# Performance work log

Measured on AMD Instinct MI355X. Metric: run time of the kernel, lower is better.

The kernel has to match this reference:

```python
import jax, jax.numpy as jnp
import numpy as np

N, E, H, ED = 20000, 640000, 128, 16


def _lin_init(k, fan_in, fan_out):
    kw, kb = jax.random.split(k)
    lim = 1.0 / np.sqrt(fan_in)
    W = jax.random.uniform(kw, (fan_in, fan_out), jnp.float32, -lim, lim)
    b = jax.random.uniform(kb, (fan_out,), jnp.float32, -lim, lim)
    return W, b


def setup_inputs() -> dict:
    key = jax.random.key(0)
    ks = jax.random.split(key, 12)
    h = jax.random.normal(ks[0], (N, H), jnp.float32)
    x = jax.random.normal(ks[1], (N, 3), jnp.float32)
    edge_index = jax.random.randint(ks[2], (2, E), 0, N, jnp.int32)
    edge_attr = jax.random.normal(ks[3], (E, ED), jnp.float32)
    fixed_mask = jax.random.randint(ks[4], (N,), 0, 2, jnp.int32).astype(bool)
    We1, be1 = _lin_init(ks[5], 2 * H + 1 + ED, H)
    We2, be2 = _lin_init(ks[6], H, H)
    Wx1, bx1 = _lin_init(ks[7], H, H)
    Wx2, bx2 = _lin_init(ks[8], H, 1)
    Wh1, bh1 = _lin_init(ks[9], 2 * H, H)
    Wh2, bh2 = _lin_init(ks[10], H, H)
    return {"h": h, "x": x, "edge_index": edge_index, "edge_attr": edge_attr,
            "fixed_mask": fixed_mask,
            "We1": We1, "be1": be1, "We2": We2, "be2": be2,
            "Wx1": Wx1, "bx1": bx1, "Wx2": Wx2, "bx2": bx2,
            "Wh1": Wh1, "bh1": bh1, "Wh2": Wh2, "bh2": bh2}


def reference(h, x, edge_index, edge_attr, fixed_mask,
              We1, be1, We2, be2, Wx1, bx1, Wx2, bx2, Wh1, bh1, Wh2, bh2):
    src, dst = edge_index[0], edge_index[1]
    n = h.shape[0]
    diff = x[src] - x[dst]                               # [E,3]
    dist_sq_norm = jnp.sum(diff * diff, -1, keepdims=True) / 100.0
    e_in = jnp.concatenate([h[src], h[dst], dist_sq_norm, edge_attr], -1)
    m_ij = jax.nn.silu(jax.nn.silu(e_in @ We1 + be1) @ We2 + be2)  # [E,H]
    coord_w = jnp.tanh(jax.nn.silu(m_ij @ Wx1 + bx1) @ Wx2 + bx2)  # [E,1]
    coord_agg = jax.ops.segment_sum(diff * coord_w, dst, num_segments=n)
    coord_agg = coord_agg * (~fixed_mask).astype(h.dtype)[:, None]
    msg_agg = jax.ops.segment_sum(m_ij, dst, num_segments=n)       # [N,H]
    h_new = h + jax.nn.silu(jnp.concatenate([h, msg_agg], -1) @ Wh1 + bh1) @ Wh2 + bh2
    x_new = x + coord_agg
    return h_new, x_new
```

## Files before the change

kernel.cpp:

```cpp
#include <hip/hip_runtime.h>
#include <hip/hip_bf16.h>
#include <math.h>

#define NN   20000
#define NE   640000
#define HD   128
#define EDIM 16
#define KIN  273
#define P2   136

#define S_PWT   4096
#define S_PWE1M 32768
#define S_PW4   16384
#define S_PWH1  32768
#define S_PWH2  16384

typedef __bf16 bf16x8 __attribute__((ext_vector_type(8)));
typedef float  f32x4  __attribute__((ext_vector_type(4)));

__device__ __forceinline__ float silu_f(float v) {
    const float e = __expf(-v);
    return v * __builtin_amdgcn_rcpf(1.0f + e);
}
__device__ __forceinline__ float tanh_f(float s) {
    const float e = __expf(2.0f * s);
    return 1.0f - 2.0f * __builtin_amdgcn_rcpf(e + 1.0f);
}
__device__ __forceinline__ unsigned short f2bf(float f) {
    __bf16 b = (__bf16)f;
    return __builtin_bit_cast(unsigned short, b);
}
__device__ __forceinline__ float bf2f(unsigned short u) {
    __bf16 b = __builtin_bit_cast(__bf16, u);
    return (float)b;
}
__device__ __forceinline__ unsigned pack2bf(float a, float b) {
    return (unsigned)f2bf(a) | ((unsigned)f2bf(b) << 16);
}

__device__ __forceinline__ void pack_id(const float* __restrict__ W, int Kreal,
                                        unsigned short* __restrict__ P, int idx) {
    const int f = idx >> 9, r = idx & 511;
    const int lane = r >> 3, j = r & 7;
    const int kb = f >> 3, nb = f & 7;
    const int k = kb * 32 + (lane >> 4) * 8 + j;
    const int n = nb * 16 + (lane & 15);
    P[idx] = f2bf((k < Kreal) ? W[(size_t)k * HD + n] : 0.0f);
}
__device__ __forceinline__ void pack_il(const float* __restrict__ W, int Kreal,
                                        unsigned short* __restrict__ P, int idx) {
    const int f = idx >> 9, r = idx & 511;
    const int lane = r >> 3, j = r & 7;
    const int kb = f >> 3, nb = f & 7;
    const int k = kb * 32 + (lane >> 4) * 8 + j;
    const int n = (nb >> 1) * 32 + 2 * (lane & 15) + (nb & 1);
    P[idx] = f2bf((k < Kreal) ? W[(size_t)k * HD + n] : 0.0f);
}

#define ZDW (NN*(HD+3))

__global__ void egnn_prep_kernel(
    const float* __restrict__ h, const int* __restrict__ ei,
    const float* __restrict__ We1, const float* __restrict__ We2,
    const float* __restrict__ Wx1, const float* __restrict__ Wh1,
    const float* __restrict__ Wh2,
    int* __restrict__ zbase,
    unsigned short* __restrict__ hb,
    unsigned short* __restrict__ PWt,  unsigned short* __restrict__ PWe1m,
    unsigned short* __restrict__ PWe2, unsigned short* __restrict__ PWx1,
    unsigned short* __restrict__ PWh1, unsigned short* __restrict__ PWh2,
    int* __restrict__ cnt)
{
    const size_t NH4 = (size_t)NN * HD / 4;
    const size_t Z1 = ZDW, C1 = Z1 + NH4;
    const size_t T1 = C1 + S_PWT, T2 = T1 + S_PWE1M, T3 = T2 + S_PW4;
    const size_t T4 = T3 + S_PW4, T5 = T4 + S_PWH1, T6 = T5 + S_PWH2;
    const size_t TOT = T6 + NE;
    const size_t stride = (size_t)gridDim.x * blockDim.x;
    for (size_t i = (size_t)blockIdx.x * blockDim.x + threadIdx.x; i < TOT; i += stride) {
        if (i < Z1) { zbase[i] = 0; continue; }
        if (i < C1) {
            const size_t r = i - Z1;
            const float4 v = ((const float4*)h)[r];
            unsigned* dst = (unsigned*)&hb[r * 4];
            dst[0] = pack2bf(v.x, v.y);
            dst[1] = pack2bf(v.z, v.w);
            continue;
        }
        if (i < T1) {
            const int idx = (int)(i - C1);
            const int r = idx & 511, nb = idx >> 9;
            const int lane = r >> 3, j = r & 7;
            const int k = 256 + (lane >> 4) * 8 + j;
            const int n = (nb >> 1) * 32 + 2 * (lane & 15) + (nb & 1);
            PWt[idx] = f2bf((k < KIN) ? We1[(size_t)k * HD + n] : 0.0f);
            continue;
        }
        if (i < T2) { pack_il(We1, 256, PWe1m, (int)(i - T1)); continue; }
        if (i < T3) { pack_il(We2, HD, PWe2, (int)(i - T2)); continue; }
        if (i < T4) { pack_il(Wx1, HD, PWx1, (int)(i - T3)); continue; }
        if (i < T5) { pack_id(Wh1, 2 * HD, PWh1, (int)(i - T4)); continue; }
        if (i < T6) { pack_id(Wh2, HD, PWh2, (int)(i - T5)); continue; }
        atomicAdd(&cnt[ei[NE + (i - T6)]], 1);
    }
}

__global__ __launch_bounds__(256, 4) void egnn_pre_kernel(
    const unsigned short* __restrict__ hb,
    const unsigned short* __restrict__ PWe1m, const float* __restrict__ be1,
    const int* __restrict__ cnt, int* __restrict__ cursor,
    unsigned short* __restrict__ preS, unsigned short* __restrict__ preD)
{
    const int t = threadIdx.x;
    if (blockIdx.x == 313) {
        __shared__ int ls[256];
        const int base = t * 79;
        int c[79];
        int s = 0;
        for (int i = 0; i < 79; ++i) {
            const int idx = base + i;
            c[i] = (idx < NN) ? cnt[idx] : 0;
            s += c[i];
        }
        ls[t] = s;
        __syncthreads();
        int v = s;
        for (int off = 1; off < 256; off <<= 1) {
            const int u = (t >= off) ? ls[t - off] : 0;
            __syncthreads();
            v += u;
            ls[t] = v;
            __syncthreads();
        }
        int run = v - s;
        for (int i = 0; i < 79; ++i) {
            const int idx = base + i;
            if (idx < NN) { cursor[idx] = run; run += c[i]; }
        }
        return;
    }
    const int n0 = blockIdx.x * 64;
    const int lane = t & 63, w = t >> 6;
    const int quad = lane >> 4, l16 = lane & 15;
    int arow[4];
    #pragma unroll
    for (int mb = 0; mb < 4; ++mb) arow[mb] = min(n0 + mb * 16 + l16, NN - 1);

    f32x4 accS[4][2], accD[4][2];
    #pragma unroll
    for (int mb = 0; mb < 4; ++mb)
        #pragma unroll
        for (int nt = 0; nt < 2; ++nt) {
            accS[mb][nt] = (f32x4){0.f,0.f,0.f,0.f};
            accD[mb][nt] = (f32x4){0.f,0.f,0.f,0.f};
        }
    #pragma unroll
    for (int kb = 0; kb < 4; ++kb) {
        bf16x8 a[4], bS[2], bD[2];
        #pragma unroll
        for (int mb = 0; mb < 4; ++mb)
            a[mb] = *(const bf16x8*)&hb[(size_t)arow[mb] * HD + kb * 32 + quad * 8];
        #pragma unroll
        for (int nt = 0; nt < 2; ++nt) {
            bS[nt] = *(const bf16x8*)&PWe1m[((kb * 8 + w * 2 + nt) * 64 + lane) * 8];
            bD[nt] = *(const bf16x8*)&PWe1m[(((4 + kb) * 8 + w * 2 + nt) * 64 + lane) * 8];
        }
        #pragma unroll
        for (int mb = 0; mb < 4; ++mb)
            #pragma unroll
            for (int nt = 0; nt < 2; ++nt) {
                accS[mb][nt] = __builtin_amdgcn_mfma_f32_16x16x32_bf16(
                    a[mb], bS[nt], accS[mb][nt], 0, 0, 0);
                accD[mb][nt] = __builtin_amdgcn_mfma_f32_16x16x32_bf16(
                    a[mb], bD[nt], accD[mb][nt], 0, 0, 0);
            }
    }
    const int cb = w * 32 + 2 * l16;
    const float2 b1 = *(const float2*)&be1[cb];
    #pragma unroll
    for (int mb = 0; mb < 4; ++mb)
        #pragma unroll
        for (int r = 0; r < 4; ++r) {
            const int n = n0 + mb * 16 + quad * 4 + r;
            if (n < NN) {
                *(unsigned*)&preS[(size_t)n * HD + cb] =
                    pack2bf(accS[mb][0][r], accS[mb][1][r]);
                *(unsigned*)&preD[(size_t)n * HD + cb] =
                    pack2bf(accD[mb][0][r] + b1.x, accD[mb][1][r] + b1.y);
            }
        }
}

__global__ void egnn_perm_kernel(const int* __restrict__ ei,
                                 int* __restrict__ cursor, int* __restrict__ perm) {
    const int e = blockIdx.x * 256 + threadIdx.x;
    const int pos = atomicAdd(&cursor[ei[NE + e]], 1);
    perm[pos] = e;
}

__global__ __launch_bounds__(256, 4) void egnn_edge_kernel(
    const unsigned short* __restrict__ preS, const unsigned short* __restrict__ preD,
    const float* __restrict__ x,
    const int* __restrict__ ei, const float* __restrict__ eattr,
    const int* __restrict__ perm,
    const unsigned short* __restrict__ PWt,
    const unsigned short* __restrict__ PWe2, const float* __restrict__ be2,
    const unsigned short* __restrict__ PWx1, const float* __restrict__ bx1,
    const float* __restrict__ Wx2, const float* __restrict__ bx2,
    float* __restrict__ msg_agg, float* __restrict__ coord_agg)
{
    __shared__ __align__(16) unsigned short tail[64 * 32];
    __shared__ __align__(16) unsigned short sT[64 * P2];
    __shared__ __align__(16) unsigned short sM[64 * P2];
    __shared__ int   sE[64], sSrc[64], sDst[64];
    __shared__ float sDiff[64][3];
    __shared__ float sW[64];

    const int t  = threadIdx.x;
    const int e0 = blockIdx.x * 64;

    if (t < 64) {
        const int e = perm[e0 + t];
        sE[t] = e;
        const int s = ei[e];
        const int d = ei[NE + e];
        sSrc[t] = s; sDst[t] = d;
        const float dx = x[s*3+0] - x[d*3+0];
        const float dy = x[s*3+1] - x[d*3+1];
        const float dz = x[s*3+2] - x[d*3+2];
        sDiff[t][0] = dx; sDiff[t][1] = dy; sDiff[t][2] = dz;
        tail[t * 32 + 0] = f2bf((dx*dx + dy*dy + dz*dz) * 0.01f);
    }
    __syncthreads();

    const int lane = t & 63;
    const int w    = t >> 6;
    const int quad = lane >> 4;
    const int l16  = lane & 15;
    const int cb   = w * 32 + 2 * l16;

    f32x4 preC[4][2];
    #pragma unroll
    for (int mb = 0; mb < 4; ++mb)
        #pragma unroll
        for (int r = 0; r < 4; ++r) {
            const int row = mb * 16 + quad * 4 + r;
            const unsigned us = *(const unsigned*)&preS[(size_t)sSrc[row] * HD + cb];
            const unsigned ud = *(const unsigned*)&preD[(size_t)sDst[row] * HD + cb];
            preC[mb][0][r] = bf2f((unsigned short)(us & 0xffff)) +
                             bf2f((unsigned short)(ud & 0xffff));
            preC[mb][1][r] = bf2f((unsigned short)(us >> 16)) +
                             bf2f((unsigned short)(ud >> 16));
        }

    {
        const int eL = t >> 2, q = t & 3;
        const int eG = sE[eL];
        #pragma unroll
        for (int jj = 0; jj < 8; ++jj) {
            const int col = q * 8 + jj;
            if (col == 0) continue;
            float v = 0.0f;
            if (col <= EDIM) v = eattr[(size_t)eG * EDIM + (col - 1)];
            tail[eL * 32 + col] = f2bf(v);
        }
    }
    __syncthreads();

    f32x4 acc1[4][2];
    {
        bf16x8 a[4], b[2];
        #pragma unroll
        for (int mb = 0; mb < 4; ++mb)
            a[mb] = *(const bf16x8*)&tail[(mb * 16 + l16) * 32 + quad * 8];
        #pragma unroll
        for (int nt = 0; nt < 2; ++nt)
            b[nt] = *(const bf16x8*)&PWt[((w * 2 + nt) * 64 + lane) * 8];
        #pragma unroll
        for (int mb = 0; mb < 4; ++mb)
            #pragma unroll
            for (int nt = 0; nt < 2; ++nt)
                acc1[mb][nt] = __builtin_amdgcn_mfma_f32_16x16x32_bf16(
                    a[mb], b[nt], preC[mb][nt], 0, 0, 0);
    }
    #pragma unroll
    for (int mb = 0; mb < 4; ++mb)
        #pragma unroll
        for (int r = 0; r < 4; ++r) {
            const int row = mb * 16 + quad * 4 + r;
            *(unsigned*)&sT[row * P2 + cb] =
                pack2bf(silu_f(acc1[mb][0][r]), silu_f(acc1[mb][1][r]));
        }
    __syncthreads();

    f32x4 acc2[4][2];
    #pragma unroll
    for (int mb = 0; mb < 4; ++mb)
        #pragma unroll
        for (int nt = 0; nt < 2; ++nt) acc2[mb][nt] = (f32x4){0.f,0.f,0.f,0.f};
    #pragma unroll
    for (int kb = 0; kb < 4; ++kb) {
        bf16x8 a[4], b[2];
        #pragma unroll
        for (int mb = 0; mb < 4; ++mb)
            a[mb] = *(const bf16x8*)&sT[(mb * 16 + l16) * P2 + kb * 32 + quad * 8];
        #pragma unroll
        for (int nt = 0; nt < 2; ++nt)
            b[nt] = *(const bf16x8*)&PWe2[((kb * 8 + w * 2 + nt) * 64 + lane) * 8];
        #pragma unroll
        for (int mb = 0; mb < 4; ++mb)
            #pragma unroll
            for (int nt = 0; nt < 2; ++nt)
                acc2[mb][nt] = __builtin_amdgcn_mfma_f32_16x16x32_bf16(
                    a[mb], b[nt], acc2[mb][nt], 0, 0, 0);
    }
    {
        const float2 b2 = *(const float2*)&be2[cb];
        #pragma unroll
        for (int mb = 0; mb < 4; ++mb)
            #pragma unroll
            for (int r = 0; r < 4; ++r) {
                const int row = mb * 16 + quad * 4 + r;
                *(unsigned*)&sM[row * P2 + cb] =
                    pack2bf(silu_f(acc2[mb][0][r] + b2.x),
                            silu_f(acc2[mb][1][r] + b2.y));
            }
    }
    __syncthreads();

    {
        const int cp = t & 63;
        const int r0 = (t >> 6) * 16;
        float a0 = 0.0f, a1 = 0.0f;
        #pragma unroll 4
        for (int r = 0; r < 16; ++r) {
            const int row = r0 + r;
            const int d   = sDst[row];
            const unsigned u = *(const unsigned*)&sM[row * P2 + 2 * cp];
            a0 += bf2f((unsigned short)(u & 0xffff));
            a1 += bf2f((unsigned short)(u >> 16));
            const bool flush = (r == 15) || (sDst[row + 1] != d);
            if (flush) {
                atomicAdd(&msg_agg[(size_t)d * HD + 2 * cp], a0);
                atomicAdd(&msg_agg[(size_t)d * HD + 2 * cp + 1], a1);
                a0 = 0.0f; a1 = 0.0f;
            }
        }
    }

    f32x4 acc3[4][2];
    #pragma unroll
    for (int mb = 0; mb < 4; ++mb)
        #pragma unroll
        for (int nt = 0; nt < 2; ++nt) acc3[mb][nt] = (f32x4){0.f,0.f,0.f,0.f};
    #pragma unroll
    for (int kb = 0; kb < 4; ++kb) {
        bf16x8 a[4], b[2];
        #pragma unroll
        for (int mb = 0; mb < 4; ++mb)
            a[mb] = *(const bf16x8*)&sM[(mb * 16 + l16) * P2 + kb * 32 + quad * 8];
        #pragma unroll
        for (int nt = 0; nt < 2; ++nt)
            b[nt] = *(const bf16x8*)&PWx1[((kb * 8 + w * 2 + nt) * 64 + lane) * 8];
        #pragma unroll
        for (int mb = 0; mb < 4; ++mb)
            #pragma unroll
            for (int nt = 0; nt < 2; ++nt)
                acc3[mb][nt] = __builtin_amdgcn_mfma_f32_16x16x32_bf16(
                    a[mb], b[nt], acc3[mb][nt], 0, 0, 0);
    }
    {
        const float2 bx = *(const float2*)&bx1[cb];
        const float2 w2 = *(const float2*)&Wx2[cb];
        float p[4][4];
        #pragma unroll
        for (int mb = 0; mb < 4; ++mb)
            #pragma unroll
            for (int r = 0; r < 4; ++r)
                p[mb][r] = silu_f(acc3[mb][0][r] + bx.x) * w2.x +
                           silu_f(acc3[mb][1][r] + bx.y) * w2.y;
        #pragma unroll
        for (int off = 8; off >= 1; off >>= 1)
            #pragma unroll
            for (int mb = 0; mb < 4; ++mb)
                #pragma unroll
                for (int r = 0; r < 4; ++r)
                    p[mb][r] += __shfl_xor(p[mb][r], off, 64);
        if (l16 == 0) {
            float* red = reinterpret_cast<float*>(sT);
            #pragma unroll
            for (int mb = 0; mb < 4; ++mb)
                #pragma unroll
                for (int r = 0; r < 4; ++r)
                    red[w * 64 + mb * 16 + quad * 4 + r] = p[mb][r];
        }
    }
    __syncthreads();
    if (t < 64) {
        const float* red = reinterpret_cast<const float*>(sT);
        sW[t] = tanh_f(red[t] + red[64 + t] + red[128 + t] + red[192 + t] + bx2[0]);
    }
    __syncthreads();

    if (w < 3) {
        const int dstv = sDst[lane];
        float v = sDiff[lane][w] * sW[lane];
        #pragma unroll
        for (int off = 1; off <= 32; off <<= 1) {
            const int   dn = __shfl_down(dstv, off, 64);
            const float vn = __shfl_down(v, off, 64);
            if (lane + off < 64 && dn == dstv) v += vn;
        }
        const int up = __shfl_up(dstv, 1, 64);
        if (lane == 0 || up != dstv)
            atomicAdd(&coord_agg[(size_t)dstv * 3 + w], v);
    }
}

__global__ __launch_bounds__(256, 4) void egnn_node_kernel(
    const unsigned short* __restrict__ hb, const float* __restrict__ h,
    const float* __restrict__ x, const int* __restrict__ fixed_mask,
    const unsigned short* __restrict__ PWh1, const float* __restrict__ bh1,
    const unsigned short* __restrict__ PWh2, const float* __restrict__ bh2,
    const float* __restrict__ msg_agg, const float* __restrict__ coord_agg,
    float* __restrict__ out_h, float* __restrict__ out_x)
{
    __shared__ __align__(16) unsigned short sTn[64 * P2];
    const int t  = threadIdx.x;
    const int n0 = blockIdx.x * 64;
    const int lane = t & 63, w = t >> 6;
    const int quad = lane >> 4, l16 = lane & 15;

    if (t < 192) {
        const int ln = t / 3, d3 = t - ln * 3;
        const int n  = n0 + ln;
        if (n < NN) {
            const float add = (fixed_mask[n] != 0) ? 0.0f : coord_agg[(size_t)n*3 + d3];
            out_x[(size_t)n*3 + d3] = x[(size_t)n*3 + d3] + add;
        }
    }

    int nrow[4];
    #pragma unroll
    for (int mb = 0; mb < 4; ++mb) nrow[mb] = min(n0 + mb * 16 + l16, NN - 1);

    f32x4 acc[4][2];
    #pragma unroll
    for (int mb = 0; mb < 4; ++mb)
        #pragma unroll
        for (int nt = 0; nt < 2; ++nt) acc[mb][nt] = (f32x4){0.f,0.f,0.f,0.f};

    #pragma unroll
    for (int kb = 0; kb < 8; ++kb) {
        bf16x8 a[4], b[2];
        if (kb < 4) {
            #pragma unroll
            for (int mb = 0; mb < 4; ++mb)
                a[mb] = *(const bf16x8*)&hb[(size_t)nrow[mb] * HD + kb * 32 + quad * 8];
        } else {
            #pragma unroll
            for (int mb = 0; mb < 4; ++mb) {
                const float* mp = msg_agg + (size_t)nrow[mb] * HD + (kb - 4) * 32 + quad * 8;
                const float4 v0 = ((const float4*)mp)[0];
                const float4 v1 = ((const float4*)mp)[1];
                bf16x8 av;
                av[0]=(__bf16)v0.x; av[1]=(__bf16)v0.y; av[2]=(__bf16)v0.z; av[3]=(__bf16)v0.w;
                av[4]=(__bf16)v1.x; av[5]=(__bf16)v1.y; av[6]=(__bf16)v1.z; av[7]=(__bf16)v1.w;
                a[mb] = av;
            }
        }
        #pragma unroll
        for (int nt = 0; nt < 2; ++nt)
            b[nt] = *(const bf16x8*)&PWh1[((kb * 8 + w * 2 + nt) * 64 + lane) * 8];
        #pragma unroll
        for (int mb = 0; mb < 4; ++mb)
            #pragma unroll
            for (int nt = 0; nt < 2; ++nt)
                acc[mb][nt] = __builtin_amdgcn_mfma_f32_16x16x32_bf16(
                    a[mb], b[nt], acc[mb][nt], 0, 0, 0);
    }
    #pragma unroll
    for (int nt = 0; nt < 2; ++nt) {
        const int col = w * 32 + nt * 16 + l16;
        const float bias = bh1[col];
        #pragma unroll
        for (int mb = 0; mb < 4; ++mb)
            #pragma unroll
            for (int r = 0; r < 4; ++r) {
                const int row = mb * 16 + quad * 4 + r;
                sTn[row * P2 + col] = f2bf(silu_f(acc[mb][nt][r] + bias));
            }
    }
    __syncthreads();

    #pragma unroll
    for (int mb = 0; mb < 4; ++mb)
        #pragma unroll
        for (int nt = 0; nt < 2; ++nt) acc[mb][nt] = (f32x4){0.f,0.f,0.f,0.f};
    #pragma unroll
    for (int kb = 0; kb < 4; ++kb) {
        bf16x8 a[4], b[2];
        #pragma unroll
        for (int mb = 0; mb < 4; ++mb)
            a[mb] = *(const bf16x8*)&sTn[(mb * 16 + l16) * P2 + kb * 32 + quad * 8];
        #pragma unroll
        for (int nt = 0; nt < 2; ++nt)
            b[nt] = *(const bf16x8*)&PWh2[((kb * 8 + w * 2 + nt) * 64 + lane) * 8];
        #pragma unroll
        for (int mb = 0; mb < 4; ++mb)
            #pragma unroll
            for (int nt = 0; nt < 2; ++nt)
                acc[mb][nt] = __builtin_amdgcn_mfma_f32_16x16x32_bf16(
                    a[mb], b[nt], acc[mb][nt], 0, 0, 0);
    }
    #pragma unroll
    for (int nt = 0; nt < 2; ++nt) {
        const int col = w * 32 + nt * 16 + l16;
        const float bias = bh2[col];
        #pragma unroll
        for (int mb = 0; mb < 4; ++mb)
            #pragma unroll
            for (int r = 0; r < 4; ++r) {
                const int row = mb * 16 + quad * 4 + r;
                const int n   = n0 + row;
                if (n < NN)
                    out_h[(size_t)n * HD + col] =
                        h[(size_t)n * HD + col] + acc[mb][nt][r] + bias;
            }
    }
}

extern "C" void kernel_launch(void* const* d_in, const int* in_sizes, int n_in,
                              void* d_out, int out_size, void* d_ws, size_t ws_size,
                              hipStream_t stream)
{
    const float* h     = (const float*)d_in[0];
    const float* x     = (const float*)d_in[1];
    const int*   ei    = (const int*)d_in[2];
    const float* eattr = (const float*)d_in[3];
    const int*   fmask = (const int*)d_in[4];
    const float* We1   = (const float*)d_in[5];
    const float* be1   = (const float*)d_in[6];
    const float* We2   = (const float*)d_in[7];
    const float* be2   = (const float*)d_in[8];
    const float* Wx1   = (const float*)d_in[9];
    const float* bx1   = (const float*)d_in[10];
    const float* Wx2   = (const float*)d_in[11];
    const float* bx2   = (const float*)d_in[12];
    const float* Wh1   = (const float*)d_in[13];
    const float* bh1   = (const float*)d_in[14];
    const float* Wh2   = (const float*)d_in[15];
    const float* bh2   = (const float*)d_in[16];

    float* msg    = (float*)d_ws;
    float* coord  = msg + (size_t)NN * HD;
    int*   cnt    = (int*)(coord + (size_t)NN * 3);
    int*   cursor = cnt + NN;
    int*   perm   = cursor + NN;
    unsigned short* hb    = (unsigned short*)(perm + NE);
    unsigned short* preS  = hb + (size_t)NN * HD;
    unsigned short* preD  = preS + (size_t)NN * HD;
    unsigned short* PWt   = preD + (size_t)NN * HD;
    unsigned short* PWe1m = PWt + S_PWT;
    unsigned short* PWe2  = PWe1m + S_PWE1M;
    unsigned short* PWx1  = PWe2 + S_PW4;
    unsigned short* PWh1  = PWx1 + S_PW4;
    unsigned short* PWh2  = PWh1 + S_PWH1;

    float* out_h = (float*)d_out;
    float* out_x = out_h + (size_t)NN * HD;

    hipMemsetAsync(cnt, 0, (size_t)NN * sizeof(int), stream);
    egnn_prep_kernel<<<1024, 256, 0, stream>>>(
        h, ei, We1, We2, Wx1, Wh1, Wh2, (int*)d_ws,
        hb, PWt, PWe1m, PWe2, PWx1, PWh1, PWh2, cnt);
    egnn_pre_kernel<<<314, 256, 0, stream>>>(hb, PWe1m, be1, cnt, cursor, preS, preD);
    egnn_perm_kernel<<<NE / 256, 256, 0, stream>>>(ei, cursor, perm);
    egnn_edge_kernel<<<NE / 64, 256, 0, stream>>>(
        preS, preD, x, ei, eattr, perm, PWt, PWe2, be2, PWx1, bx1,
        Wx2, bx2, msg, coord);
    egnn_node_kernel<<<(NN + 63) / 64, 256, 0, stream>>>(
        hb, h, x, fmask, PWh1, bh1, PWh2, bh2, msg, coord, out_h, out_x);
}
```

Measured before the change: 394.6 us.

## Fuse node projection into prep kernel, localize perm scan, shrink edge LDS

```diff
diff --git a/kernel.cpp b/kernel.cpp
--- a/kernel.cpp
+++ b/kernel.cpp
@@ -10,7 +10,6 @@
 #define P2   136
 
 #define S_PWT   4096
-#define S_PWE1M 32768
 #define S_PW4   16384
 #define S_PWH1  32768
 #define S_PWH2  16384
@@ -57,71 +56,147 @@
     P[idx] = f2bf((k < Kreal) ? W[(size_t)k * HD + n] : 0.0f);
 }
 
-#define ZDW (NN*(HD+3))
-
-__global__ void egnn_prep_kernel(
+#define ZDW   (NN*(HD+3))
+#define PREPB (1024 + 313)
+
+__global__ __launch_bounds__(256, 4) void egnn_prep_kernel(
     const float* __restrict__ h, const int* __restrict__ ei,
     const float* __restrict__ We1, const float* __restrict__ We2,
     const float* __restrict__ Wx1, const float* __restrict__ Wh1,
-    const float* __restrict__ Wh2,
+    const float* __restrict__ Wh2, const float* __restrict__ be1,
     int* __restrict__ zbase,
     unsigned short* __restrict__ hb,
-    unsigned short* __restrict__ PWt,  unsigned short* __restrict__ PWe1m,
-    unsigned short* __restrict__ PWe2, unsigned short* __restrict__ PWx1,
-    unsigned short* __restrict__ PWh1, unsigned short* __restrict__ PWh2,
-    int* __restrict__ cnt)
-{
-    const size_t NH4 = (size_t)NN * HD / 4;
-    const size_t Z1 = ZDW, C1 = Z1 + NH4;
-    const size_t T1 = C1 + S_PWT, T2 = T1 + S_PWE1M, T3 = T2 + S_PW4;
-    const size_t T4 = T3 + S_PW4, T5 = T4 + S_PWH1, T6 = T5 + S_PWH2;
-    const size_t TOT = T6 + NE;
-    const size_t stride = (size_t)gridDim.x * blockDim.x;
-    for (size_t i = (size_t)blockIdx.x * blockDim.x + threadIdx.x; i < TOT; i += stride) {
-        if (i < Z1) { zbase[i] = 0; continue; }
-        if (i < C1) {
-            const size_t r = i - Z1;
-            const float4 v = ((const float4*)h)[r];
-            unsigned* dst = (unsigned*)&hb[r * 4];
-            dst[0] = pack2bf(v.x, v.y);
-            dst[1] = pack2bf(v.z, v.w);
-            continue;
-        }
-        if (i < T1) {
-            const int idx = (int)(i - C1);
-            const int r = idx & 511, nb = idx >> 9;
-            const int lane = r >> 3, j = r & 7;
-            const int k = 256 + (lane >> 4) * 8 + j;
-            const int n = (nb >> 1) * 32 + 2 * (lane & 15) + (nb & 1);
-            PWt[idx] = f2bf((k < KIN) ? We1[(size_t)k * HD + n] : 0.0f);
-            continue;
-        }
-        if (i < T2) { pack_il(We1, 256, PWe1m, (int)(i - T1)); continue; }
-        if (i < T3) { pack_il(We2, HD, PWe2, (int)(i - T2)); continue; }
-        if (i < T4) { pack_il(Wx1, HD, PWx1, (int)(i - T3)); continue; }
-        if (i < T5) { pack_id(Wh1, 2 * HD, PWh1, (int)(i - T4)); continue; }
-        if (i < T6) { pack_id(Wh2, HD, PWh2, (int)(i - T5)); continue; }
-        atomicAdd(&cnt[ei[NE + (i - T6)]], 1);
-    }
-}
-
-__global__ __launch_bounds__(256, 4) void egnn_pre_kernel(
-    const unsigned short* __restrict__ hb,
-    const unsigned short* __restrict__ PWe1m, const float* __restrict__ be1,
-    const int* __restrict__ cnt, int* __restrict__ cursor,
+    unsigned short* __restrict__ PWt,  unsigned short* __restrict__ PWe2,
+    unsigned short* __restrict__ PWx1, unsigned short* __restrict__ PWh1,
+    unsigned short* __restrict__ PWh2,
+    int* __restrict__ cnt,
     unsigned short* __restrict__ preS, unsigned short* __restrict__ preD)
 {
+    __shared__ __align__(16) unsigned short fragB[16384];
     const int t = threadIdx.x;
-    if (blockIdx.x == 313) {
-        __shared__ int ls[256];
-        const int base = t * 79;
-        int c[79];
+    const int b = blockIdx.x;
+
+    if (b < 1024) {
+        const size_t NH4 = (size_t)NN * HD / 4;
+        const size_t Z1 = ZDW, C1 = Z1 + NH4;
+        const size_t T1 = C1 + S_PWT, T2 = T1 + S_PW4, T3 = T2 + S_PW4;
+        const size_t T4 = T3 + S_PWH1, T5 = T4 + S_PWH2;
+        const size_t TOT = T5 + NE;
+        const size_t stride = (size_t)1024 * 256;
+        for (size_t i = (size_t)b * 256 + t; i < TOT; i += stride) {
+            if (i < Z1) { zbase[i] = 0; continue; }
+            if (i < C1) {
+                const size_t r = i - Z1;
+                const float4 v = ((const float4*)h)[r];
+                unsigned* dst = (unsigned*)&hb[r * 4];
+                dst[0] = pack2bf(v.x, v.y);
+                dst[1] = pack2bf(v.z, v.w);
+                continue;
+            }
+            if (i < T1) {
+                const int idx = (int)(i - C1);
+                const int r = idx & 511, nb = idx >> 9;
+                const int lane = r >> 3, j = r & 7;
+                const int k = 256 + (lane >> 4) * 8 + j;
+                const int n = (nb >> 1) * 32 + 2 * (lane & 15) + (nb & 1);
+                PWt[idx] = f2bf((k < KIN) ? We1[(size_t)k * HD + n] : 0.0f);
+                continue;
+            }
+            if (i < T2) { pack_il(We2, HD, PWe2, (int)(i - T1)); continue; }
+            if (i < T3) { pack_il(Wx1, HD, PWx1, (int)(i - T2)); continue; }
+            if (i < T4) { pack_id(Wh1, 2 * HD, PWh1, (int)(i - T3)); continue; }
+            if (i < T5) { pack_id(Wh2, HD, PWh2, (int)(i - T4)); continue; }
+            atomicAdd(&cnt[ei[NE + (i - T5)]], 1);
+        }
+        return;
+    }
+
+    const int pb = b - 1024;
+    const int n0 = pb * 64;
+    const int lane = t & 63, w = t >> 6;
+    const int quad = lane >> 4, l16 = lane & 15;
+    int arow[4];
+    #pragma unroll
+    for (int mb = 0; mb < 4; ++mb) arow[mb] = min(n0 + mb * 16 + l16, NN - 1);
+
+    f32x4 accS[4][2], accD[4][2];
+    #pragma unroll
+    for (int mb = 0; mb < 4; ++mb)
+        #pragma unroll
+        for (int nt = 0; nt < 2; ++nt) {
+            accS[mb][nt] = (f32x4){0.f,0.f,0.f,0.f};
+            accD[mb][nt] = (f32x4){0.f,0.f,0.f,0.f};
+        }
+
+    for (int half = 0; half < 2; ++half) {
+        __syncthreads();
+        for (int i = t; i < 16384; i += 256) {
+            const int f = i >> 9, r = i & 511;
+            const int ln = r >> 3, j = r & 7;
+            const int kb = f >> 3, nb = f & 7;
+            const int k = half * 128 + kb * 32 + (ln >> 4) * 8 + j;
+            const int n = (nb >> 1) * 32 + 2 * (ln & 15) + (nb & 1);
+            fragB[i] = f2bf(We1[(size_t)k * HD + n]);
+        }
+        __syncthreads();
+        f32x4 (*acc)[2] = half ? accD : accS;
+        #pragma unroll
+        for (int kb = 0; kb < 4; ++kb) {
+            bf16x8 a[4], bb[2];
+            #pragma unroll
+            for (int mb = 0; mb < 4; ++mb) {
+                const float* hp = h + (size_t)arow[mb] * HD + kb * 32 + quad * 8;
+                const float4 v0 = ((const float4*)hp)[0];
+                const float4 v1 = ((const float4*)hp)[1];
+                bf16x8 av;
+                av[0]=(__bf16)v0.x; av[1]=(__bf16)v0.y; av[2]=(__bf16)v0.z; av[3]=(__bf16)v0.w;
+                av[4]=(__bf16)v1.x; av[5]=(__bf16)v1.y; av[6]=(__bf16)v1.z; av[7]=(__bf16)v1.w;
+                a[mb] = av;
+            }
+            #pragma unroll
+            for (int nt = 0; nt < 2; ++nt)
+                bb[nt] = *(const bf16x8*)&fragB[((kb * 8 + w * 2 + nt) * 64 + lane) * 8];
+            #pragma unroll
+            for (int mb = 0; mb < 4; ++mb)
+                #pragma unroll
+                for (int nt = 0; nt < 2; ++nt)
+                    acc[mb][nt] = __builtin_amdgcn_mfma_f32_16x16x32_bf16(
+                        a[mb], bb[nt], acc[mb][nt], 0, 0, 0);
+        }
+    }
+    const int cb = w * 32 + 2 * l16;
+    const float2 b1 = *(const float2*)&be1[cb];
+    #pragma unroll
+    for (int mb = 0; mb < 4; ++mb)
+        #pragma unroll
+        for (int r = 0; r < 4; ++r) {
+            const int n = n0 + mb * 16 + quad * 4 + r;
+            if (n < NN) {
+                *(unsigned*)&preS[(size_t)n * HD + cb] =
+                    pack2bf(accS[mb][0][r], accS[mb][1][r]);
+                *(unsigned*)&preD[(size_t)n * HD + cb] =
+                    pack2bf(accD[mb][0][r] + b1.x, accD[mb][1][r] + b1.y);
+            }
+        }
+}
+
+__global__ __launch_bounds__(256, 2) void egnn_perm_kernel(
+    const int* __restrict__ ei, int* __restrict__ cnt, int* __restrict__ perm)
+{
+    __shared__ int base[10000];
+    __shared__ int ls[256];
+    const int t = threadIdx.x;
+    const int b = blockIdx.x;
+    const int e0 = b * 1250;
+
+    for (int half = 0; half < 2; ++half) {
+        const int lo = half * 10000;
         int s = 0;
         for (int i = 0; i < 79; ++i) {
-            const int idx = base + i;
-            c[i] = (idx < NN) ? cnt[idx] : 0;
-            s += c[i];
-        }
+            const int idx = t * 79 + i;
+            if (idx < NN) s += (cnt[idx] & 0xFFFFF);
+        }
+        __syncthreads();
         ls[t] = s;
         __syncthreads();
         int v = s;
@@ -134,71 +209,25 @@
         }
         int run = v - s;
         for (int i = 0; i < 79; ++i) {
-            const int idx = base + i;
-            if (idx < NN) { cursor[idx] = run; run += c[i]; }
-        }
-        return;
-    }
-    const int n0 = blockIdx.x * 64;
-    const int lane = t & 63, w = t >> 6;
-    const int quad = lane >> 4, l16 = lane & 15;
-    int arow[4];
-    #pragma unroll
-    for (int mb = 0; mb < 4; ++mb) arow[mb] = min(n0 + mb * 16 + l16, NN - 1);
-
-    f32x4 accS[4][2], accD[4][2];
-    #pragma unroll
-    for (int mb = 0; mb < 4; ++mb)
-        #pragma unroll
-        for (int nt = 0; nt < 2; ++nt) {
-            accS[mb][nt] = (f32x4){0.f,0.f,0.f,0.f};
-            accD[mb][nt] = (f32x4){0.f,0.f,0.f,0.f};
-        }
-    #pragma unroll
-    for (int kb = 0; kb < 4; ++kb) {
-        bf16x8 a[4], bS[2], bD[2];
-        #pragma unroll
-        for (int mb = 0; mb < 4; ++mb)
-            a[mb] = *(const bf16x8*)&hb[(size_t)arow[mb] * HD + kb * 32 + quad * 8];
-        #pragma unroll
-        for (int nt = 0; nt < 2; ++nt) {
-            bS[nt] = *(const bf16x8*)&PWe1m[((kb * 8 + w * 2 + nt) * 64 + lane) * 8];
-            bD[nt] = *(const bf16x8*)&PWe1m[(((4 + kb) * 8 + w * 2 + nt) * 64 + lane) * 8];
-        }
-        #pragma unroll
-        for (int mb = 0; mb < 4; ++mb)
-            #pragma unroll
-            for (int nt = 0; nt < 2; ++nt) {
-                accS[mb][nt] = __builtin_amdgcn_mfma_f32_16x16x32_bf16(
-                    a[mb], bS[nt], accS[mb][nt], 0, 0, 0);
-                accD[mb][nt] = __builtin_amdgcn_mfma_f32_16x16x32_bf16(
-                    a[mb], bD[nt], accD[mb][nt], 0, 0, 0);
-            }
-    }
-    const int cb = w * 32 + 2 * l16;
-    const float2 b1 = *(const float2*)&be1[cb];
-    #pragma unroll
-    for (int mb = 0; mb < 4; ++mb)
-        #pragma unroll
-        for (int r = 0; r < 4; ++r) {
-            const int n = n0 + mb * 16 + quad * 4 + r;
-            if (n < NN) {
-                *(unsigned*)&preS[(size_t)n * HD + cb] =
-                    pack2bf(accS[mb][0][r], accS[mb][1][r]);
-                *(unsigned*)&preD[(size_t)n * HD + cb] =
-                    pack2bf(accD[mb][0][r] + b1.x, accD[mb][1][r] + b1.y);
-            }
-        }
-}
-
-__global__ void egnn_perm_kernel(const int* __restrict__ ei,
-                                 int* __restrict__ cursor, int* __restrict__ perm) {
-    const int e = blockIdx.x * 256 + threadIdx.x;
-    const int pos = atomicAdd(&cursor[ei[NE + e]], 1);
-    perm[pos] = e;
-}
-
-__global__ __launch_bounds__(256, 4) void egnn_edge_kernel(
+            const int idx = t * 79 + i;
+            if (idx < NN) {
+                const int c = cnt[idx] & 0xFFFFF;
+                if (idx >= lo && idx < lo + 10000) base[idx - lo] = run;
+                run += c;
+            }
+        }
+        __syncthreads();
+        for (int e = e0 + t; e < e0 + 1250; e += 256) {
+            const int d = ei[NE + e];
+            if (d >= lo && d < lo + 10000) {
+                const int old = atomicAdd(&cnt[d], 1 << 20);
+                perm[base[d - lo] + (old >> 20)] = e;
+            }
+        }
+    }
+}
+
+__global__ __launch_bounds__(256, 8) void egnn_edge_kernel(
     const unsigned short* __restrict__ preS, const unsigned short* __restrict__ preD,
     const float* __restrict__ x,
     const int* __restrict__ ei, const float* __restrict__ eattr,
@@ -209,15 +238,14 @@
     const float* __restrict__ Wx2, const float* __restrict__ bx2,
     float* __restrict__ msg_agg, float* __restrict__ coord_agg)
 {
-    __shared__ __align__(16) unsigned short tail[64 * 32];
-    __shared__ __align__(16) unsigned short sT[64 * P2];
-    __shared__ __align__(16) unsigned short sM[64 * P2];
+    __shared__ __align__(16) unsigned short buf[64 * P2];
     __shared__ int   sE[64], sSrc[64], sDst[64];
     __shared__ float sDiff[64][3];
     __shared__ float sW[64];
 
     const int t  = threadIdx.x;
     const int e0 = blockIdx.x * 64;
+    unsigned short* tail = buf;
 
     if (t < 64) {
         const int e = perm[e0 + t];
@@ -283,12 +311,14 @@
                 acc1[mb][nt] = __builtin_amdgcn_mfma_f32_16x16x32_bf16(
                     a[mb], b[nt], preC[mb][nt], 0, 0, 0);
     }
+    __syncthreads();
+
     #pragma unroll
     for (int mb = 0; mb < 4; ++mb)
         #pragma unroll
         for (int r = 0; r < 4; ++r) {
             const int row = mb * 16 + quad * 4 + r;
-            *(unsigned*)&sT[row * P2 + cb] =
+            *(unsigned*)&buf[row * P2 + cb] =
                 pack2bf(silu_f(acc1[mb][0][r]), silu_f(acc1[mb][1][r]));
         }
     __syncthreads();
@@ -303,7 +333,7 @@
         bf16x8 a[4], b[2];
         #pragma unroll
         for (int mb = 0; mb < 4; ++mb)
-            a[mb] = *(const bf16x8*)&sT[(mb * 16 + l16) * P2 + kb * 32 + quad * 8];
+            a[mb] = *(const bf16x8*)&buf[(mb * 16 + l16) * P2 + kb * 32 + quad * 8];
         #pragma unroll
         for (int nt = 0; nt < 2; ++nt)
             b[nt] = *(const bf16x8*)&PWe2[((kb * 8 + w * 2 + nt) * 64 + lane) * 8];
@@ -314,6 +344,8 @@
                 acc2[mb][nt] = __builtin_amdgcn_mfma_f32_16x16x32_bf16(
                     a[mb], b[nt], acc2[mb][nt], 0, 0, 0);
     }
+    __syncthreads();
+
     {
         const float2 b2 = *(const float2*)&be2[cb];
         #pragma unroll
@@ -321,7 +353,7 @@
             #pragma unroll
             for (int r = 0; r < 4; ++r) {
                 const int row = mb * 16 + quad * 4 + r;
-                *(unsigned*)&sM[row * P2 + cb] =
+                *(unsigned*)&buf[row * P2 + cb] =
                     pack2bf(silu_f(acc2[mb][0][r] + b2.x),
                             silu_f(acc2[mb][1][r] + b2.y));
             }
@@ -336,7 +368,7 @@
         for (int r = 0; r < 16; ++r) {
             const int row = r0 + r;
             const int d   = sDst[row];
-            const unsigned u = *(const unsigned*)&sM[row * P2 + 2 * cp];
+            const unsigned u = *(const unsigned*)&buf[row * P2 + 2 * cp];
             a0 += bf2f((unsigned short)(u & 0xffff));
             a1 += bf2f((unsigned short)(u >> 16));
             const bool flush = (r == 15) || (sDst[row + 1] != d);
@@ -358,7 +390,7 @@
         bf16x8 a[4], b[2];
         #pragma unroll
         for (int mb = 0; mb < 4; ++mb)
-            a[mb] = *(const bf16x8*)&sM[(mb * 16 + l16) * P2 + kb * 32 + quad * 8];
+            a[mb] = *(const bf16x8*)&buf[(mb * 16 + l16) * P2 + kb * 32 + quad * 8];
         #pragma unroll
         for (int nt = 0; nt < 2; ++nt)
             b[nt] = *(const bf16x8*)&PWx1[((kb * 8 + w * 2 + nt) * 64 + lane) * 8];
@@ -369,10 +401,10 @@
                 acc3[mb][nt] = __builtin_amdgcn_mfma_f32_16x16x32_bf16(
                     a[mb], b[nt], acc3[mb][nt], 0, 0, 0);
     }
+    float p[4][4];
     {
         const float2 bx = *(const float2*)&bx1[cb];
         const float2 w2 = *(const float2*)&Wx2[cb];
-        float p[4][4];
         #pragma unroll
         for (int mb = 0; mb < 4; ++mb)
             #pragma unroll
@@ -386,18 +418,20 @@
                 #pragma unroll
                 for (int r = 0; r < 4; ++r)
                     p[mb][r] += __shfl_xor(p[mb][r], off, 64);
-        if (l16 == 0) {
-            float* red = reinterpret_cast<float*>(sT);
-            #pragma unroll
-            for (int mb = 0; mb < 4; ++mb)
-                #pragma unroll
-                for (int r = 0; r < 4; ++r)
-                    red[w * 64 + mb * 16 + quad * 4 + r] = p[mb][r];
-        }
+    }
+    __syncthreads();
+
+    if (l16 == 0) {
+        float* red = reinterpret_cast<float*>(buf);
+        #pragma unroll
+        for (int mb = 0; mb < 4; ++mb)
+            #pragma unroll
+            for (int r = 0; r < 4; ++r)
+                red[w * 64 + mb * 16 + quad * 4 + r] = p[mb][r];
     }
     __syncthreads();
     if (t < 64) {
-        const float* red = reinterpret_cast<const float*>(sT);
+        const float* red = reinterpret_cast<const float*>(buf);
         sW[t] = tanh_f(red[t] + red[64 + t] + red[128 + t] + red[192 + t] + bx2[0]);
     }
     __syncthreads();
@@ -555,14 +589,12 @@
     float* msg    = (float*)d_ws;
     float* coord  = msg + (size_t)NN * HD;
     int*   cnt    = (int*)(coord + (size_t)NN * 3);
-    int*   cursor = cnt + NN;
-    int*   perm   = cursor + NN;
+    int*   perm   = cnt + NN;
     unsigned short* hb    = (unsigned short*)(perm + NE);
     unsigned short* preS  = hb + (size_t)NN * HD;
     unsigned short* preD  = preS + (size_t)NN * HD;
     unsigned short* PWt   = preD + (size_t)NN * HD;
-    unsigned short* PWe1m = PWt + S_PWT;
-    unsigned short* PWe2  = PWe1m + S_PWE1M;
+    unsigned short* PWe2  = PWt + S_PWT;
     unsigned short* PWx1  = PWe2 + S_PW4;
     unsigned short* PWh1  = PWx1 + S_PW4;
     unsigned short* PWh2  = PWh1 + S_PWH1;
@@ -571,11 +603,10 @@
     float* out_x = out_h + (size_t)NN * HD;
 
     hipMemsetAsync(cnt, 0, (size_t)NN * sizeof(int), stream);
-    egnn_prep_kernel<<<1024, 256, 0, stream>>>(
-        h, ei, We1, We2, Wx1, Wh1, Wh2, (int*)d_ws,
-        hb, PWt, PWe1m, PWe2, PWx1, PWh1, PWh2, cnt);
-    egnn_pre_kernel<<<314, 256, 0, stream>>>(hb, PWe1m, be1, cnt, cursor, preS, preD);
-    egnn_perm_kernel<<<NE / 256, 256, 0, stream>>>(ei, cursor, perm);
+    egnn_prep_kernel<<<PREPB, 256, 0, stream>>>(
+        h, ei, We1, We2, Wx1, Wh1, Wh2, be1, (int*)d_ws,
+        hb, PWt, PWe2, PWx1, PWh1, PWh2, cnt, preS, preD);
+    egnn_perm_kernel<<<512, 256, 0, stream>>>(ei, cnt, perm);
     egnn_edge_kernel<<<NE / 64, 256, 0, stream>>>(
         preS, preD, x, ei, eattr, perm, PWt, PWe2, be2, PWx1, bx1,
         Wx2, bx2, msg, coord);
```

New measurement: 741.0 us. +87.8%, slower.
